# Kernel tuning notes

Hardware: AMD Instinct MI355X
Metric: run time of the kernel (lower is better)

## Reference

```python
import jax, jax.numpy as jnp
import numpy as np

B, T, C, H, L, V = 2, 1024, 768, 12, 6, 32000
HS = C // H  # head size 64
EPS = 1e-5


def _ln(x, g, b):
    m = jnp.mean(x, axis=-1, keepdims=True)
    v = jnp.var(x, axis=-1, keepdims=True)
    return (x - m) * jax.lax.rsqrt(v + EPS) * g + b


def setup_inputs() -> dict:
    key = jax.random.key(0)
    ks = iter(jax.random.split(key, 32))
    s = lambda *sh: jax.random.normal(next(ks), sh, jnp.float32) * 0.02
    return {
        "idx": jax.random.randint(next(ks), (B, T), 0, V),
        "tok_emb": s(V, C),
        "pos_emb": s(T, C),
        "Wq": s(L, H, C, HS), "Wk": s(L, H, C, HS), "Wv": s(L, H, C, HS),
        "Wp": s(L, C, C), "bp": jnp.zeros((L, C), jnp.float32),
        "ln1g": jnp.ones((L, C), jnp.float32), "ln1b": jnp.zeros((L, C), jnp.float32),
        "ln2g": jnp.ones((L, C), jnp.float32), "ln2b": jnp.zeros((L, C), jnp.float32),
        "W1": s(L, C, 4 * C), "b1": jnp.zeros((L, 4 * C), jnp.float32),
        "W2": s(L, 4 * C, C), "b2": jnp.zeros((L, C), jnp.float32),
        "lnfg": jnp.ones((C,), jnp.float32), "lnfb": jnp.zeros((C,), jnp.float32),
        "Wh": s(C, V), "bh": jnp.zeros((V,), jnp.float32),
    }


def reference(idx, tok_emb, pos_emb, Wq, Wk, Wv, Wp, bp, ln1g, ln1b, ln2g, ln2b,
              W1, b1, W2, b2, lnfg, lnfb, Wh, bh):
    x = tok_emb[idx] + pos_emb[None, :, :]  # [B,T,C]
    # NOTE: original scales by full embed dim C ** -0.5 (not head_size)
    scale = C ** (-0.5)
    causal = jnp.tril(jnp.ones((T, T), bool))

    def block(x, p):
        wq, wk, wv, wp, bpj, g1, be1, g2, be2, w1, bb1, w2, bb2 = p
        h = _ln(x, g1, be1)
        q = jnp.einsum('btc,hcs->bhts', h, wq)
        k = jnp.einsum('btc,hcs->bhts', h, wk)
        v = jnp.einsum('btc,hcs->bhts', h, wv)
        wei = jnp.einsum('bhts,bhus->bhtu', q, k) * scale
        wei = jnp.where(causal, wei, -jnp.inf)
        wei = jax.nn.softmax(wei, axis=-1)
        o = jnp.einsum('bhtu,bhus->bhts', wei, v)
        o = o.transpose(0, 2, 1, 3).reshape(x.shape[0], T, C)  # concat heads
        x = x + o @ wp + bpj
        h2 = _ln(x, g2, be2)
        x = x + jax.nn.relu(h2 @ w1 + bb1) @ w2 + bb2
        return x, None

    x, _ = jax.lax.scan(block, x, (Wq, Wk, Wv, Wp, bp, ln1g, ln1b, ln2g, ln2b, W1, b1, W2, b2))
    logits = _ln(x, lnfg, lnfb) @ Wh + bh  # [B,T,V]
    return logits
```

## Files before the change

### kernel.cpp

```cpp
#include <hip/hip_runtime.h>

#define B_ 2
#define T_ 1024
#define C_ 768
#define H_ 12
#define L_ 6
#define V_ 32000
#define HS_ 64
#define M_ (B_*T_)
#define C4_ (4*C_)
#define NVC_ 6400

typedef __attribute__((ext_vector_type(8))) short short8;
typedef __attribute__((ext_vector_type(4))) float f32x4;

__device__ __forceinline__ float b2f(unsigned short u) {
  union { unsigned int i; float f; } x; x.i = ((unsigned int)u) << 16; return x.f;
}
__device__ __forceinline__ unsigned short f2b(float f) {
  unsigned int u = __builtin_bit_cast(unsigned int, f);
  u += 0x7fffu + ((u >> 16) & 1u);
  return (unsigned short)(u >> 16);
}

__device__ __forceinline__ void gload16(const unsigned short* g, unsigned short* l) {
  __builtin_amdgcn_global_load_lds(
      (const __attribute__((address_space(1))) unsigned int*)g,
      (__attribute__((address_space(3))) unsigned int*)l, 16, 0, 0);
}

__global__ __launch_bounds__(256) void transpose_f2b(const float* __restrict__ in,
                                                     unsigned short* __restrict__ out,
                                                     int ldi, int ldo, size_t zi, size_t zo) {
  __shared__ unsigned short tile[32][33];
  in  += zi * blockIdx.z;
  out += zo * blockIdx.z;
  int c0 = blockIdx.x * 32, r0 = blockIdx.y * 32;
  int tx = threadIdx.x & 31, ty = threadIdx.x >> 5;
  #pragma unroll
  for (int j = 0; j < 32; j += 8)
    tile[ty + j][tx] = f2b(in[(size_t)(r0 + ty + j) * ldi + c0 + tx]);
  __syncthreads();
  #pragma unroll
  for (int j = 0; j < 32; j += 8)
    out[(size_t)(c0 + ty + j) * ldo + r0 + tx] = tile[tx][ty + j];
}

__global__ __launch_bounds__(256) void transpose_qkvp(const float* __restrict__ Wq,
                                                      const float* __restrict__ Wk,
                                                      const float* __restrict__ Wv,
                                                      const float* __restrict__ Wp,
                                                      unsigned short* __restrict__ out) {
  __shared__ unsigned short tile[32][33];
  int z = blockIdx.z;
  const float* in; unsigned short* o; int ldi; int cbase;
  if (z < 36) {
    int which = z / H_, hh = z % H_;
    in = (which == 0 ? Wq : which == 1 ? Wk : Wv) + (size_t)hh * C_ * HS_;
    o = out + (size_t)which * C_ * C_ + (size_t)hh * HS_ * C_;
    ldi = HS_; cbase = 0;
  } else {
    int ch = z - 36;
    in = Wp; ldi = C_; cbase = ch * 64;
    o = out + (size_t)3 * C_ * C_ + (size_t)ch * 64 * C_;
  }
  int c0 = blockIdx.x * 32, r0 = blockIdx.y * 32;
  int tx = threadIdx.x & 31, ty = threadIdx.x >> 5;
  #pragma unroll
  for (int j = 0; j < 32; j += 8)
    tile[ty + j][tx] = f2b(in[(size_t)(r0 + ty + j) * ldi + cbase + c0 + tx]);
  __syncthreads();
  #pragma unroll
  for (int j = 0; j < 32; j += 8)
    o[(size_t)(c0 + ty + j) * C_ + r0 + tx] = tile[tx][ty + j];
}

__global__ __launch_bounds__(256) void embed_kernel(const int* __restrict__ idx,
                                                    const float* __restrict__ tok,
                                                    const float* __restrict__ pos,
                                                    float* __restrict__ x) {
  int m = blockIdx.x;
  int t = m & (T_ - 1);
  int tk = idx[m];
  #pragma unroll
  for (int i = 0; i < 3; ++i) {
    int c = threadIdx.x + i * 256;
    x[(size_t)m * C_ + c] = tok[(size_t)tk * C_ + c] + pos[(size_t)t * C_ + c];
  }
}

__global__ __launch_bounds__(256) void ln_kernel(const float* __restrict__ x,
                                                 const float* __restrict__ g,
                                                 const float* __restrict__ bta,
                                                 unsigned short* __restrict__ h) {
  int wave = threadIdx.x >> 6, lane = threadIdx.x & 63;
  int m = blockIdx.x * 4 + wave;
  const float* xr = x + (size_t)m * C_;
  float v[12], s = 0.f, ss = 0.f;
  #pragma unroll
  for (int i = 0; i < 12; ++i) {
    v[i] = xr[lane + i * 64];
    s += v[i]; ss += v[i] * v[i];
  }
  #pragma unroll
  for (int off = 32; off; off >>= 1) { s += __shfl_xor(s, off); ss += __shfl_xor(ss, off); }
  float mean = s * (1.f / C_);
  float var  = fmaxf(ss * (1.f / C_) - mean * mean, 0.f);
  float rstd = rsqrtf(var + 1e-5f);
  #pragma unroll
  for (int i = 0; i < 12; ++i) {
    int c = lane + i * 64;
    h[(size_t)m * C_ + c] = f2b((v[i] - mean) * rstd * g[c] + bta[c]);
  }
}

__global__ __launch_bounds__(256) void attn_mfma(const unsigned short* __restrict__ q,
                                                 const unsigned short* __restrict__ k,
                                                 const unsigned short* __restrict__ v,
                                                 unsigned short* __restrict__ o) {
  const float scale = 0.03608439182435161f;
  __shared__ __align__(16) unsigned short Ks[64 * 72];
  __shared__ __align__(16) unsigned short Vt[64 * 72];
  __shared__ __align__(16) unsigned short Ps[4][16 * 72];

  int tid = threadIdx.x;
  int lane = tid & 63, wave = tid >> 6;
  int rl = lane & 15, kgrp = lane >> 4, koff = kgrp * 8;
  int bh = blockIdx.y;
  int hh = bh % H_, bb = bh / H_;
  size_t base = (size_t)bb * T_ * C_ + (size_t)hh * HS_;

  for (int pass = 0; pass < 2; ++pass) {
    int qt = pass ? (15 - (int)blockIdx.x) : (int)blockIdx.x;

    short8 qf0 = *(const short8*)&q[base + (size_t)(qt * 64 + wave * 16 + rl) * C_ + koff];
    short8 qf1 = *(const short8*)&q[base + (size_t)(qt * 64 + wave * 16 + rl) * C_ + 32 + koff];

    float m_[4], l_[4];
    f32x4 oacc[4];
    #pragma unroll
    for (int r = 0; r < 4; ++r) { m_[r] = -INFINITY; l_[r] = 0.f; }
    #pragma unroll
    for (int j = 0; j < 4; ++j) oacc[j] = (f32x4){0.f, 0.f, 0.f, 0.f};

    short8 kreg[2], vreg[2];
    #pragma unroll
    for (int i = 0; i < 2; ++i) {
      int e = tid + i * 256;
      kreg[i] = *(const short8*)&k[base + (size_t)(e >> 3) * C_ + (e & 7) * 8];
      vreg[i] = *(const short8*)&v[base + (size_t)(e >> 3) * C_ + (e & 7) * 8];
    }

    for (int kt = 0; kt <= qt; ++kt) {
      #pragma unroll
      for (int i = 0; i < 2; ++i) {
        int e = tid + i * 256, row = e >> 3, c8 = e & 7;
        *(short8*)&Ks[row * 72 + c8 * 8] = kreg[i];
      }
      #pragma unroll
      for (int i = 0; i < 2; ++i) {
        int e = tid + i * 256, kk = e >> 3, d8 = (e & 7) * 8;
        short8 vv = vreg[i];
        #pragma unroll
        for (int t2 = 0; t2 < 8; ++t2) {
          int ii = (t2 + tid) & 7;
          Vt[(d8 + ii) * 72 + kk] = vv[ii];
        }
      }
      __syncthreads();

      if (kt < qt) {
        #pragma unroll
        for (int i = 0; i < 2; ++i) {
          int e = tid + i * 256;
          kreg[i] = *(const short8*)&k[base + (size_t)((kt + 1) * 64 + (e >> 3)) * C_ + (e & 7) * 8];
          vreg[i] = *(const short8*)&v[base + (size_t)((kt + 1) * 64 + (e >> 3)) * C_ + (e & 7) * 8];
        }
      }

      f32x4 s[4];
      #pragma unroll
      for (int j = 0; j < 4; ++j) s[j] = (f32x4){0.f, 0.f, 0.f, 0.f};
      __builtin_amdgcn_s_setprio(1);
      #pragma unroll
      for (int j = 0; j < 4; ++j) {
        short8 b0 = *(const short8*)&Ks[(j * 16 + rl) * 72 + koff];
        short8 b1 = *(const short8*)&Ks[(j * 16 + rl) * 72 + 32 + koff];
        s[j] = __builtin_amdgcn_mfma_f32_16x16x32_bf16(qf0, b0, s[j], 0, 0, 0);
        s[j] = __builtin_amdgcn_mfma_f32_16x16x32_bf16(qf1, b1, s[j], 0, 0, 0);
      }
      __builtin_amdgcn_s_setprio(0);

      bool diag = (kt == qt);
      #pragma unroll
      for (int j = 0; j < 4; ++j)
        #pragma unroll
        for (int r = 0; r < 4; ++r) {
          float sv = s[j][r] * scale;
          if (diag) {
            int urow = j * 16 + rl, qrow = wave * 16 + kgrp * 4 + r;
            if (urow > qrow) sv = -INFINITY;
          }
          s[j][r] = sv;
        }

      float corr[4], rs[4];
      #pragma unroll
      for (int r = 0; r < 4; ++r) {
        float mrow = fmaxf(fmaxf(s[0][r], s[1][r]), fmaxf(s[2][r], s[3][r]));
        #pragma unroll
        for (int off = 8; off; off >>= 1) mrow = fmaxf(mrow, __shfl_xor(mrow, off));
        float mnew = fmaxf(m_[r], mrow);
        corr[r] = __expf(m_[r] - mnew);
        m_[r] = mnew;
      }
      #pragma unroll
      for (int r = 0; r < 4; ++r) rs[r] = 0.f;
      #pragma unroll
      for (int j = 0; j < 4; ++j)
        #pragma unroll
        for (int r = 0; r < 4; ++r) {
          float p = (s[j][r] == -INFINITY) ? 0.f : __expf(s[j][r] - m_[r]);
          s[j][r] = p;
          rs[r] += p;
        }
      #pragma unroll
      for (int r = 0; r < 4; ++r) {
        #pragma unroll
        for (int off = 8; off; off >>= 1) rs[r] += __shfl_xor(rs[r], off);
        l_[r] = l_[r] * corr[r] + rs[r];
      }
      #pragma unroll
      for (int j = 0; j < 4; ++j)
        #pragma unroll
        for (int r = 0; r < 4; ++r) oacc[j][r] *= corr[r];

      #pragma unroll
      for (int j = 0; j < 4; ++j)
        #pragma unroll
        for (int r = 0; r < 4; ++r)
          Ps[wave][(kgrp * 4 + r) * 72 + j * 16 + rl] = f2b(s[j][r]);

      short8 pa0 = *(const short8*)&Ps[wave][rl * 72 + koff];
      short8 pa1 = *(const short8*)&Ps[wave][rl * 72 + 32 + koff];
      __builtin_amdgcn_s_setprio(1);
      #pragma unroll
      for (int j = 0; j < 4; ++j) {
        short8 b0 = *(const short8*)&Vt[(j * 16 + rl) * 72 + koff];
        short8 b1 = *(const short8*)&Vt[(j * 16 + rl) * 72 + 32 + koff];
        oacc[j] = __builtin_amdgcn_mfma_f32_16x16x32_bf16(pa0, b0, oacc[j], 0, 0, 0);
        oacc[j] = __builtin_amdgcn_mfma_f32_16x16x32_bf16(pa1, b1, oacc[j], 0, 0, 0);
      }
      __builtin_amdgcn_s_setprio(0);
      __syncthreads();
    }

    #pragma unroll
    for (int j = 0; j < 4; ++j)
      #pragma unroll
      for (int r = 0; r < 4; ++r) {
        int qrow = wave * 16 + kgrp * 4 + r;
        o[base + (size_t)(qt * 64 + qrow) * C_ + j * 16 + rl] = f2b(oacc[j][r] / l_[r]);
      }
  }
}

template<int BM, int BN, int EPI, bool MFAST, bool SWZ>
__global__ __launch_bounds__(256) void gemm_bt(const unsigned short* __restrict__ A,
                                               const unsigned short* __restrict__ Bt,
                                               const float* __restrict__ bias,
                                               unsigned short* __restrict__ outb,
                                               float* __restrict__ outf,
                                               int M, int N, int K, int ldO,
                                               size_t zBt, size_t zOut, int nMt) {
  constexpr int BK = 64;
  __shared__ __align__(16) unsigned short As[BM * BK];
  __shared__ __align__(16) unsigned short Bs[BN * BK];
  constexpr int FM = BM / 32, FN = BN / 32;

  int tid = threadIdx.x;
  int lane = tid & 63, wave = tid >> 6;
  int wr = wave >> 1, wc = wave & 1;
  int m0, n0;
  if (SWZ) {
    int nwg = gridDim.x, wg = blockIdx.x;
    int qq = nwg >> 3, rr = nwg & 7;
    int xcd = wg & 7, off = wg >> 3;
    int wgid = (xcd < rr ? xcd * (qq + 1) : rr * (qq + 1) + (xcd - rr) * qq) + off;
    m0 = (wgid % nMt) * BM;
    n0 = (wgid / nMt) * BN;
  } else {
    m0 = (MFAST ? blockIdx.x : blockIdx.y) * BM;
    n0 = (MFAST ? blockIdx.y : blockIdx.x) * BN;
  }
  int rl = lane & 15, kgrp = lane >> 4;
  Bt += zBt * blockIdx.z;

  int srow = lane >> 3;
  int scol = ((lane & 7) ^ srow) * 8;

  int pc0 = ((kgrp)     ^ (rl & 7)) * 8;
  int pc1 = ((4 + kgrp) ^ (rl & 7)) * 8;

  f32x4 acc[FM][FN] = {};

  for (int k0 = 0; k0 < K; k0 += BK) {
    #pragma unroll
    for (int i = 0; i < BM / 32; ++i) {
      int r = i * 32 + wave * 8;
      gload16(&A[(size_t)(m0 + r + srow) * K + k0 + scol], &As[r * BK]);
    }
    #pragma unroll
    for (int i = 0; i < BN / 32; ++i) {
      int r = i * 32 + wave * 8;
      gload16(&Bt[(size_t)(n0 + r + srow) * K + k0 + scol], &Bs[r * BK]);
    }
    __syncthreads();

    short8 af0[FM], af1[FM], bf0[FN], bf1[FN];
    #pragma unroll
    for (int i = 0; i < FM; ++i) {
      int row = wr * (BM / 2) + i * 16 + rl;
      af0[i] = *(const short8*)&As[row * BK + pc0];
      af1[i] = *(const short8*)&As[row * BK + pc1];
    }
    #pragma unroll
    for (int j = 0; j < FN; ++j) {
      int row = wc * (BN / 2) + j * 16 + rl;
      bf0[j] = *(const short8*)&Bs[row * BK + pc0];
      bf1[j] = *(const short8*)&Bs[row * BK + pc1];
    }
    #pragma unroll
    for (int i = 0; i < FM; ++i)
      #pragma unroll
      for (int j = 0; j < FN; ++j) {
        acc[i][j] = __builtin_amdgcn_mfma_f32_16x16x32_bf16(af0[i], bf0[j], acc[i][j], 0, 0, 0);
        acc[i][j] = __builtin_amdgcn_mfma_f32_16x16x32_bf16(af1[i], bf1[j], acc[i][j], 0, 0, 0);
      }
    __syncthreads();
  }

  int rbase = kgrp * 4;
  #pragma unroll
  for (int i = 0; i < FM; ++i) {
    #pragma unroll
    for (int j = 0; j < FN; ++j) {
      #pragma unroll
      for (int r = 0; r < 4; ++r) {
        int m = m0 + wr * (BM / 2) + i * 16 + rbase + r;
        int n = n0 + wc * (BN / 2) + j * 16 + rl;
        float val = acc[i][j][r];
        if (bias) val += bias[n];
        if (EPI == 0)      (outb + zOut * blockIdx.z)[(size_t)m * ldO + n] = f2b(val);
        else if (EPI == 1) (outb + zOut * blockIdx.z)[(size_t)m * ldO + n] = f2b(fmaxf(val, 0.f));
        else if (EPI == 2) (outf + zOut * blockIdx.z)[(size_t)m * ldO + n] += val;
        else               (outf + zOut * blockIdx.z)[(size_t)m * ldO + n] = val;
      }
    }
  }
}

extern "C" void kernel_launch(void* const* d_in, const int* in_sizes, int n_in,
                              void* d_out, int out_size, void* d_ws, size_t ws_size,
                              hipStream_t stream) {
  const int*   idx  = (const int*)d_in[0];
  const float* tok  = (const float*)d_in[1];
  const float* pos  = (const float*)d_in[2];
  const float* Wq   = (const float*)d_in[3];
  const float* Wk   = (const float*)d_in[4];
  const float* Wv   = (const float*)d_in[5];
  const float* Wp   = (const float*)d_in[6];
  const float* bp   = (const float*)d_in[7];
  const float* ln1g = (const float*)d_in[8];
  const float* ln1b = (const float*)d_in[9];
  const float* ln2g = (const float*)d_in[10];
  const float* ln2b = (const float*)d_in[11];
  const float* W1   = (const float*)d_in[12];
  const float* b1   = (const float*)d_in[13];
  const float* W2   = (const float*)d_in[14];
  const float* b2   = (const float*)d_in[15];
  const float* lnfg = (const float*)d_in[16];
  const float* lnfb = (const float*)d_in[17];
  const float* Wh   = (const float*)d_in[18];
  const float* bh   = (const float*)d_in[19];

  float* out = (float*)d_out;

  const size_t MC = (size_t)M_ * C_;
  const size_t fixed = MC*4 + MC*2 + MC*2*4;
  const size_t need_chunk = fixed + (size_t)NVC_*C_*2;
  const size_t need_full  = fixed + (size_t)V_*C_*2;
  if (ws_size < need_chunk) return;
  const bool full_head = (ws_size >= need_full);

  char* p = (char*)d_ws;
  float*          x   = (float*)p;            p += MC*4;
  unsigned short* h   = (unsigned short*)p;   p += MC*2;
  unsigned short* qb  = (unsigned short*)p;   p += MC*2;
  unsigned short* kb  = (unsigned short*)p;   p += MC*2;
  unsigned short* vb  = (unsigned short*)p;   p += MC*2;
  unsigned short* ob  = (unsigned short*)p;   p += MC*2;
  unsigned short* WT  = (unsigned short*)p;
  unsigned short* mid = qb;

  unsigned short* WqT = WT;
  unsigned short* WpT = WT + (size_t)3*C_*C_;
  unsigned short* W12T = WT;

  embed_kernel<<<M_, 256, 0, stream>>>(idx, tok, pos, x);

  for (int l = 0; l < L_; ++l) {
    size_t wo  = (size_t)l * C_ * C_;
    size_t wo4 = (size_t)l * C_ * C4_;
    size_t woq = (size_t)l * H_ * C_ * HS_;

    transpose_qkvp<<<dim3(HS_/32, C_/32, 48), 256, 0, stream>>>(Wq + woq, Wk + woq, Wv + woq, Wp + wo, WqT);

    ln_kernel<<<M_/4, 256, 0, stream>>>(x, ln1g + (size_t)l*C_, ln1b + (size_t)l*C_, h);
    gemm_bt<64,64,0,false,false><<<dim3(C_/64, M_/64, 3), 256, 0, stream>>>(h, WqT, nullptr, qb, nullptr,
                                                                            M_, C_, C_, C_, (size_t)C_*C_, MC, 0);
    attn_mfma<<<dim3(8, B_*H_), 256, 0, stream>>>(qb, kb, vb, ob);
    gemm_bt<64,64,2,false,false><<<dim3(C_/64, M_/64), 256, 0, stream>>>(ob, WpT, bp + (size_t)l*C_, nullptr, x,
                                                                         M_, C_, C_, C_, 0, 0, 0);

    ln_kernel<<<M_/4, 256, 0, stream>>>(x, ln2g + (size_t)l*C_, ln2b + (size_t)l*C_, h);
    transpose_f2b<<<dim3(C4_/32, C_/32, 1), 256, 0, stream>>>(W1 + wo4, W12T, C4_, C_, 0, 0);
    gemm_bt<128,128,1,true,true><<<dim3((M_/128)*(C4_/128)), 256, 0, stream>>>(h, W12T, b1 + (size_t)l*C4_, mid, nullptr,
                                                                               M_, C4_, C_, C4_, 0, 0, M_/128);
    transpose_f2b<<<dim3(C_/32, C4_/32, 1), 256, 0, stream>>>(W2 + wo4, W12T, C_, C4_, 0, 0);
    gemm_bt<64,64,2,true,true><<<dim3((M_/64)*(C_/64)), 256, 0, stream>>>(mid, W12T, b2 + (size_t)l*C_, nullptr, x,
                                                                          M_, C_, C4_, C_, 0, 0, M_/64);
  }

  ln_kernel<<<M_/4, 256, 0, stream>>>(x, lnfg, lnfb, h);
  if (full_head) {
    transpose_f2b<<<dim3(V_/32, C_/32, 1), 256, 0, stream>>>(Wh, WT, V_, C_, 0, 0);
    gemm_bt<128,128,3,true,true><<<dim3((M_/128)*(V_/128)), 256, 0, stream>>>(
        h, WT, bh, nullptr, out, M_, V_, C_, V_, 0, 0, M_/128);
  } else {
    for (int ci = 0; ci < V_/NVC_; ++ci) {
      transpose_f2b<<<dim3(NVC_/32, C_/32, 1), 256, 0, stream>>>(Wh + (size_t)ci*NVC_, WT, V_, C_, 0, 0);
      gemm_bt<128,128,3,true,true><<<dim3((M_/128)*(NVC_/128)), 256, 0, stream>>>(
          h, WT, bh + (size_t)ci*NVC_, nullptr, out + (size_t)ci*NVC_, M_, NVC_, C_, V_, 0, 0, M_/128);
    }
  }
}
```

Measured before the change: 1.212 ms.

## Double-buffer GEMM shared-memory tiles to overlap global loads with MFMA

The GEMM kernel now keeps two LDS buffers for the A and B tiles. It issues the global-to-LDS loads for the next K tile before reading fragments and running the MFMAs on the current tile, which removes one barrier per iteration and hides load latency. It also raises wave priority around the MFMA block with s_setprio. The cost is double the LDS footprint, which can lower occupancy, and correctness now depends on gload16 being asynchronous but still completing before the next barrier.

```diff
diff --git a/kernel.cpp b/kernel.cpp
--- a/kernel.cpp
+++ b/kernel.cpp
@@ -274,8 +274,8 @@
                                                int M, int N, int K, int ldO,
                                                size_t zBt, size_t zOut, int nMt) {
   constexpr int BK = 64;
-  __shared__ __align__(16) unsigned short As[BM * BK];
-  __shared__ __align__(16) unsigned short Bs[BN * BK];
+  __shared__ __align__(16) unsigned short As[2][BM * BK];
+  __shared__ __align__(16) unsigned short Bs[2][BN * BK];
   constexpr int FM = BM / 32, FN = BN / 32;
 
   int tid = threadIdx.x;
@@ -303,33 +303,50 @@
   int pc1 = ((4 + kgrp) ^ (rl & 7)) * 8;
 
   f32x4 acc[FM][FN] = {};
-
-  for (int k0 = 0; k0 < K; k0 += BK) {
-    #pragma unroll
-    for (int i = 0; i < BM / 32; ++i) {
-      int r = i * 32 + wave * 8;
-      gload16(&A[(size_t)(m0 + r + srow) * K + k0 + scol], &As[r * BK]);
-    }
-    #pragma unroll
-    for (int i = 0; i < BN / 32; ++i) {
-      int r = i * 32 + wave * 8;
-      gload16(&Bt[(size_t)(n0 + r + srow) * K + k0 + scol], &Bs[r * BK]);
-    }
-    __syncthreads();
+  const int nt = K / BK;
+
+  #pragma unroll
+  for (int i = 0; i < BM / 32; ++i) {
+    int r = i * 32 + wave * 8;
+    gload16(&A[(size_t)(m0 + r + srow) * K + scol], &As[0][r * BK]);
+  }
+  #pragma unroll
+  for (int i = 0; i < BN / 32; ++i) {
+    int r = i * 32 + wave * 8;
+    gload16(&Bt[(size_t)(n0 + r + srow) * K + scol], &Bs[0][r * BK]);
+  }
+  __syncthreads();
+
+  int cur = 0;
+  for (int t = 0; t < nt; ++t) {
+    if (t + 1 < nt) {
+      int k0 = (t + 1) * BK;
+      #pragma unroll
+      for (int i = 0; i < BM / 32; ++i) {
+        int r = i * 32 + wave * 8;
+        gload16(&A[(size_t)(m0 + r + srow) * K + k0 + scol], &As[cur ^ 1][r * BK]);
+      }
+      #pragma unroll
+      for (int i = 0; i < BN / 32; ++i) {
+        int r = i * 32 + wave * 8;
+        gload16(&Bt[(size_t)(n0 + r + srow) * K + k0 + scol], &Bs[cur ^ 1][r * BK]);
+      }
+    }
 
     short8 af0[FM], af1[FM], bf0[FN], bf1[FN];
     #pragma unroll
     for (int i = 0; i < FM; ++i) {
       int row = wr * (BM / 2) + i * 16 + rl;
-      af0[i] = *(const short8*)&As[row * BK + pc0];
-      af1[i] = *(const short8*)&As[row * BK + pc1];
+      af0[i] = *(const short8*)&As[cur][row * BK + pc0];
+      af1[i] = *(const short8*)&As[cur][row * BK + pc1];
     }
     #pragma unroll
     for (int j = 0; j < FN; ++j) {
       int row = wc * (BN / 2) + j * 16 + rl;
-      bf0[j] = *(const short8*)&Bs[row * BK + pc0];
-      bf1[j] = *(const short8*)&Bs[row * BK + pc1];
-    }
+      bf0[j] = *(const short8*)&Bs[cur][row * BK + pc0];
+      bf1[j] = *(const short8*)&Bs[cur][row * BK + pc1];
+    }
+    __builtin_amdgcn_s_setprio(1);
     #pragma unroll
     for (int i = 0; i < FM; ++i)
       #pragma unroll
@@ -337,7 +354,9 @@
         acc[i][j] = __builtin_amdgcn_mfma_f32_16x16x32_bf16(af0[i], bf0[j], acc[i][j], 0, 0, 0);
         acc[i][j] = __builtin_amdgcn_mfma_f32_16x16x32_bf16(af1[i], bf1[j], acc[i][j], 0, 0, 0);
       }
+    __builtin_amdgcn_s_setprio(0);
     __syncthreads();
+    cur ^= 1;
   }
 
   int rbase = kgrp * 4;
```

Result: no change. 1.225 ms (+1.1%).
